# Optimization experiments

Hardware: AMD Instinct MI355X
Metric: run time of the kernel (lower is better)

Reference implementation:

```python
import jax, jax.numpy as jnp
import numpy as np

N = 50000       # nodes
E = 800000      # edges
D_IN, D_H, D_OUT = 64, 64, 32


def _glorot(key, fan_in, fan_out):
    lim = np.sqrt(6.0 / (fan_in + fan_out)).astype(np.float32)
    return jax.random.uniform(key, (fan_in, fan_out), jnp.float32, -lim, lim)


def setup_inputs() -> dict:
    key = jax.random.key(0)
    k = jax.random.split(key, 4)
    x = jax.random.normal(k[0], (N, D_IN), jnp.float32)
    edge_index = jax.random.randint(k[1], (2, E), 0, N, dtype=jnp.int64)
    W1 = _glorot(k[2], D_IN, D_H)
    b1 = jnp.zeros((D_H,), jnp.float32)
    W2 = _glorot(k[3], D_H, D_OUT)
    b2 = jnp.zeros((D_OUT,), jnp.float32)
    return {"x": x, "edge_index": edge_index, "W1": W1, "b1": b1, "W2": W2, "b2": b2}


def gcn_layer(x, W, b, src, dst, n):
    # PyG GCNConv: h = XW; add self-loops (weight 1); symmetric normalization
    # out[j] = sum_{i->j} h[i] / sqrt(deg(i) deg(j)) + h[j]/deg(j) + b
    h = x @ W                                           # [n, d_out]
    deg = jax.ops.segment_sum(jnp.ones((src.shape[0],), h.dtype), dst,
                              num_segments=n) + 1.0     # in-degree + self-loop
    dinv = jax.lax.rsqrt(deg)                           # deg >= 1
    norm = (dinv[src] * dinv[dst])[:, None]             # [E, 1]
    agg = jax.ops.segment_sum(h[src] * norm, dst, num_segments=n)
    # self-loop contribution: dinv[i]*dinv[i]*h[i]
    return agg + h * (dinv * dinv)[:, None] + b


def reference(x, edge_index, W1, b1, W2, b2):
    src, dst = edge_index[0], edge_index[1]
    h = gcn_layer(x, W1, b1, src, dst, N)
    h = jax.nn.relu(h)                                  # dropout is identity in eval mode
    return gcn_layer(h, W2, b2, src, dst, N)
```

## Files before the change

### kernel.cpp

```cpp
#include <hip/hip_runtime.h>
#include <hip/hip_fp16.h>
#include <cstddef>
#include <cstdint>

namespace {

constexpr int N  = 50000;
constexpr int E  = 800000;
constexpr int DH = 64;
constexpr int DO = 32;
constexpr int NB = (N + 255) / 256;
static_assert(N < 65536, "src packed as u16");
static_assert(NB <= 256, "phase-B single tile");

__device__ inline float bf2f(uint16_t u) {
    union { uint32_t u; float f; } c; c.u = (uint32_t)u << 16; return c.f;
}
__device__ inline uint16_t f2bf(float f) {
    union { float f; uint32_t u; } c; c.f = f;
    uint32_t r = c.u + 0x7FFFu + ((c.u >> 16) & 1u);
    return (uint16_t)(r >> 16);
}
__device__ inline void bf2x(uint32_t p, float& a, float& b) {
    union { uint32_t u; float f; } c0, c1;
    c0.u = p << 16; c1.u = p & 0xFFFF0000u;
    a = c0.f; b = c1.f;
}

__global__ void k_zero(int* __restrict__ cnt) {
    int i = blockIdx.x * blockDim.x + threadIdx.x;
    if (i < N) cnt[i] = 0;
}

__global__ void k_count(const int* __restrict__ dst, int* __restrict__ cnt,
                        int* __restrict__ rank) {
    int e = blockIdx.x * blockDim.x + threadIdx.x;
    if (e < E) rank[e] = atomicAdd(&cnt[dst[e]], 1);
}

__global__ void k_scanA(const int* __restrict__ cnt, int* __restrict__ incl,
                        int* __restrict__ bsum) {
    __shared__ int ts[256];
    const int t = threadIdx.x;
    const int i = blockIdx.x * 256 + t;
    const int v = (i < N) ? cnt[i] : 0;
    ts[t] = v;
    __syncthreads();
#pragma unroll
    for (int off = 1; off < 256; off <<= 1) {
        const int u = (t >= off) ? ts[t - off] : 0;
        __syncthreads();
        ts[t] += u;
        __syncthreads();
    }
    if (i < N) incl[i] = ts[t];
    if (t == 255) bsum[blockIdx.x] = ts[255];
}

__global__ void k_scanB(int* __restrict__ bsum) {
    __shared__ int ts[256];
    const int t = threadIdx.x;
    const int v = (t < NB) ? bsum[t] : 0;
    ts[t] = v;
    __syncthreads();
#pragma unroll
    for (int off = 1; off < 256; off <<= 1) {
        const int u = (t >= off) ? ts[t - off] : 0;
        __syncthreads();
        ts[t] += u;
        __syncthreads();
    }
    if (t < NB) bsum[t] = ts[t] - v;
}

__global__ void k_scanC(const int* __restrict__ cnt, const int* __restrict__ incl,
                        const int* __restrict__ bbase, int* __restrict__ rowptr,
                        float* __restrict__ dinv) {
    const int i = blockIdx.x * 256 + threadIdx.x;
    if (i >= N) return;
    const int c    = cnt[i];
    const int excl = bbase[blockIdx.x] + incl[i] - c;
    rowptr[i] = excl;
    dinv[i]   = rsqrtf((float)(c + 1));
    if (i == N - 1) rowptr[N] = excl + c;
}

__global__ void k_fill(const int* __restrict__ src, const int* __restrict__ dst,
                       const int* __restrict__ rank, const int* __restrict__ rowptr,
                       const float* __restrict__ dinv, uint32_t* __restrict__ epack) {
    int e = blockIdx.x * blockDim.x + threadIdx.x;
    if (e >= E) return;
    const int s = src[e], d = dst[e];
    const int pos = rowptr[d] + rank[e];
    const float wn = dinv[s] * dinv[d];
    const uint16_t hb = __half_as_ushort(__float2half(wn));
    epack[pos] = (uint32_t)s | ((uint32_t)hb << 16);
}

template <int DOUT, typename OutT>
__launch_bounds__(256)
__global__ void k_gemm(const float* __restrict__ X, const float* __restrict__ W,
                       OutT* __restrict__ H) {
    constexpr int CPT = DOUT / 16;
    static_assert(CPT == 4 || CPT == 2, "geometry");
    constexpr int XS = 68;
    __shared__ float Ws[64 * DOUT];
    __shared__ float Xs[64 * XS];

    const int tid = threadIdx.x;
    const int rowBase = blockIdx.x * 64;

    constexpr int WF4 = 64 * DOUT / 4;
#pragma unroll
    for (int i = 0; i < WF4 / 256; ++i) {
        const int q = tid + i * 256;
        reinterpret_cast<float4*>(Ws)[q] = reinterpret_cast<const float4*>(W)[q];
    }
#pragma unroll
    for (int i = 0; i < 4; ++i) {
        const int q   = tid + i * 256;
        const int row = q >> 4;
        const int kq  = q & 15;
        const int gr  = min(rowBase + row, N - 1);
        const float4 v = *reinterpret_cast<const float4*>(X + (size_t)gr * 64 + kq * 4);
        *reinterpret_cast<float4*>(&Xs[row * XS + kq * 4]) = v;
    }
    __syncthreads();

    const int rg = tid >> 4;
    const int cg = tid & 15;

    float acc[4][CPT];
#pragma unroll
    for (int r = 0; r < 4; ++r)
#pragma unroll
        for (int c = 0; c < CPT; ++c) acc[r][c] = 0.0f;

#pragma unroll
    for (int k4 = 0; k4 < 16; ++k4) {
        const int k = k4 * 4;
        float xr[4][4];
#pragma unroll
        for (int r = 0; r < 4; ++r) {
            const float4 v = *reinterpret_cast<const float4*>(&Xs[(rg * 4 + r) * XS + k]);
            xr[r][0] = v.x; xr[r][1] = v.y; xr[r][2] = v.z; xr[r][3] = v.w;
        }
#pragma unroll
        for (int i = 0; i < 4; ++i) {
            float wv[CPT];
            if constexpr (CPT == 4) {
                const float4 v = *reinterpret_cast<const float4*>(&Ws[(k + i) * DOUT + cg * 4]);
                wv[0] = v.x; wv[1] = v.y; wv[2] = v.z; wv[3] = v.w;
            } else {
                const float2 v = *reinterpret_cast<const float2*>(&Ws[(k + i) * DOUT + cg * 2]);
                wv[0] = v.x; wv[1] = v.y;
            }
#pragma unroll
            for (int r = 0; r < 4; ++r)
#pragma unroll
                for (int c = 0; c < CPT; ++c) acc[r][c] += xr[r][i] * wv[c];
        }
    }

#pragma unroll
    for (int r = 0; r < 4; ++r) {
        const int row = rowBase + rg * 4 + r;
        if (row < N) {
            if constexpr (sizeof(OutT) == 2) {
                uint2 o;
                o.x = (uint32_t)f2bf(acc[r][0]) | ((uint32_t)f2bf(acc[r][1]) << 16);
                o.y = (uint32_t)f2bf(acc[r][2]) | ((uint32_t)f2bf(acc[r][3]) << 16);
                *reinterpret_cast<uint2*>(&H[(size_t)row * DOUT + cg * 4]) = o;
            } else {
                float2 o; o.x = acc[r][0]; o.y = acc[r][1];
                *reinterpret_cast<float2*>(&H[(size_t)row * DOUT + cg * 2]) = o;
            }
        }
    }
}

__global__ void k_agg1(const int* __restrict__ rowptr, const uint32_t* __restrict__ epack,
                       const uint16_t* __restrict__ h1, const float* __restrict__ dinv,
                       const float* __restrict__ b1, float* __restrict__ y1) {
    const int gtid = blockIdx.x * blockDim.x + threadIdx.x;
    const int n    = gtid >> 6;
    const int lane = gtid & 63;
    if (n >= N) return;
    const int g  = lane >> 3;
    const int sl = lane & 7;
    const int beg = rowptr[n], end = rowptr[n + 1];

    float acc[8] = {0.f, 0.f, 0.f, 0.f, 0.f, 0.f, 0.f, 0.f};
    for (int j = beg; j < end; j += 8) {
        const int jj = j + g;
        int s = 0; float wn = 0.0f;
        if (jj < end) {
            const uint32_t w = epack[jj];
            s  = (int)(w & 0xFFFFu);
            wn = __half2float(__ushort_as_half((uint16_t)(w >> 16)));
        }
        const uint4 v = *reinterpret_cast<const uint4*>(h1 + (size_t)s * DH + sl * 8);
        float f0, f1;
        bf2x(v.x, f0, f1); acc[0] += wn * f0; acc[1] += wn * f1;
        bf2x(v.y, f0, f1); acc[2] += wn * f0; acc[3] += wn * f1;
        bf2x(v.z, f0, f1); acc[4] += wn * f0; acc[5] += wn * f1;
        bf2x(v.w, f0, f1); acc[6] += wn * f0; acc[7] += wn * f1;
    }
#pragma unroll
    for (int m = 8; m < 64; m <<= 1)
#pragma unroll
        for (int k = 0; k < 8; ++k) acc[k] += __shfl_xor(acc[k], m);

    if (g < 2) {
        const float di = dinv[n], d2 = di * di;
        const int fb = sl * 8 + g * 4;
        const uint2 sv = *reinterpret_cast<const uint2*>(h1 + (size_t)n * DH + fb);
        float s0, s1, s2, s3;
        bf2x(sv.x, s0, s1); bf2x(sv.y, s2, s3);
        const float4 bv = *reinterpret_cast<const float4*>(b1 + fb);
        float4 o;
        o.x = fmaxf(acc[g * 4 + 0] + s0 * d2 + bv.x, 0.f);
        o.y = fmaxf(acc[g * 4 + 1] + s1 * d2 + bv.y, 0.f);
        o.z = fmaxf(acc[g * 4 + 2] + s2 * d2 + bv.z, 0.f);
        o.w = fmaxf(acc[g * 4 + 3] + s3 * d2 + bv.w, 0.f);
        *reinterpret_cast<float4*>(y1 + (size_t)n * DH + fb) = o;
    }
}

__global__ void k_agg2(const int* __restrict__ rowptr, const uint32_t* __restrict__ epack,
                       const float* __restrict__ h2, const float* __restrict__ dinv,
                       const float* __restrict__ b2, float* __restrict__ out) {
    const int gtid = blockIdx.x * blockDim.x + threadIdx.x;
    const int n    = gtid >> 6;
    const int lane = gtid & 63;
    if (n >= N) return;
    const int g  = lane >> 3;
    const int sl = lane & 7;
    const int beg = rowptr[n], end = rowptr[n + 1];

    float acc[4] = {0.f, 0.f, 0.f, 0.f};
    for (int j = beg; j < end; j += 8) {
        const int jj = j + g;
        int s = 0; float wn = 0.0f;
        if (jj < end) {
            const uint32_t w = epack[jj];
            s  = (int)(w & 0xFFFFu);
            wn = __half2float(__ushort_as_half((uint16_t)(w >> 16)));
        }
        const float4 v = *reinterpret_cast<const float4*>(h2 + (size_t)s * DO + sl * 4);
        acc[0] += wn * v.x; acc[1] += wn * v.y;
        acc[2] += wn * v.z; acc[3] += wn * v.w;
    }
#pragma unroll
    for (int m = 8; m < 64; m <<= 1)
#pragma unroll
        for (int k = 0; k < 4; ++k) acc[k] += __shfl_xor(acc[k], m);

    if (g == 0) {
        const float di = dinv[n], d2 = di * di;
        const float4 sv = *reinterpret_cast<const float4*>(h2 + (size_t)n * DO + sl * 4);
        const float4 bv = *reinterpret_cast<const float4*>(b2 + sl * 4);
        float4 o;
        o.x = acc[0] + sv.x * d2 + bv.x;
        o.y = acc[1] + sv.y * d2 + bv.y;
        o.z = acc[2] + sv.z * d2 + bv.z;
        o.w = acc[3] + sv.w * d2 + bv.w;
        *reinterpret_cast<float4*>(out + (size_t)n * DO + sl * 4) = o;
    }
}

template <typename T>
T* alignp(char*& p, size_t count) {
    uintptr_t u = ((uintptr_t)p + 63) & ~(uintptr_t)63;
    p = (char*)(u + count * sizeof(T));
    return (T*)u;
}

}

extern "C" void kernel_launch(void* const* d_in, const int* in_sizes, int n_in,
                              void* d_out, int out_size, void* d_ws, size_t ws_size,
                              hipStream_t stream) {
    const float* x   = (const float*)d_in[0];
    const int*   ei  = (const int*)d_in[1];
    const float* W1  = (const float*)d_in[2];
    const float* b1  = (const float*)d_in[3];
    const float* W2  = (const float*)d_in[4];
    const float* b2  = (const float*)d_in[5];
    float* out = (float*)d_out;

    const int* src = ei;
    const int* dst = ei + E;

    char* p = (char*)d_ws;
    int*      cnt    = alignp<int>(p, N);
    int*      rowptr = alignp<int>(p, N + 1);
    int*      rank   = alignp<int>(p, E);
    float*    dinv   = alignp<float>(p, N);
    int*      incl   = alignp<int>(p, N);
    int*      bsum   = alignp<int>(p, NB);
    uint32_t* epack  = alignp<uint32_t>(p, E);
    uint16_t* h1     = alignp<uint16_t>(p, (size_t)N * DH);
    float*    y1     = alignp<float>(p, (size_t)N * DH);
    float*    h2     = (float*)h1;

    hipLaunchKernelGGL(k_zero, dim3((N + 255) / 256), dim3(256), 0, stream, cnt);
    hipLaunchKernelGGL(k_count, dim3((E + 255) / 256), dim3(256), 0, stream,
                       dst, cnt, rank);
    hipLaunchKernelGGL(k_scanA, dim3(NB), dim3(256), 0, stream, cnt, incl, bsum);
    hipLaunchKernelGGL(k_scanB, dim3(1), dim3(256), 0, stream, bsum);
    hipLaunchKernelGGL(k_scanC, dim3(NB), dim3(256), 0, stream, cnt, incl, bsum,
                       rowptr, dinv);
    hipLaunchKernelGGL(k_fill, dim3((E + 255) / 256), dim3(256), 0, stream,
                       src, dst, rank, rowptr, dinv, epack);
    hipLaunchKernelGGL((k_gemm<DH, uint16_t>), dim3((N + 63) / 64), dim3(256), 0, stream,
                       x, W1, h1);
    hipLaunchKernelGGL(k_agg1, dim3((N * 64 + 255) / 256), dim3(256), 0, stream,
                       rowptr, epack, h1, dinv, b1, y1);
    hipLaunchKernelGGL((k_gemm<DO, float>), dim3((N + 63) / 64), dim3(256), 0, stream,
                       y1, W2, h2);
    hipLaunchKernelGGL(k_agg2, dim3((N * 64 + 255) / 256), dim3(256), 0, stream,
                       rowptr, epack, h2, dinv, b2, out);
}
```

Measured before the change: 160.0 us.

## Fuse GEMM1 into count kernel, fuse layer-2 GEMM into agg1, bf16 h2

New measurement: 156.3 us. -2.3%, faster.

```diff
diff --git a/kernel.cpp b/kernel.cpp
--- a/kernel.cpp
+++ b/kernel.cpp
@@ -10,12 +10,14 @@
 constexpr int DH = 64;
 constexpr int DO = 32;
 constexpr int NB = (N + 255) / 256;
+constexpr int CB = (E + 255) / 256;
+constexpr int GB = (N + 63) / 64;
+constexpr int A1B = 3136;
+constexpr int NPW = 4;
 static_assert(N < 65536, "src packed as u16");
 static_assert(NB <= 256, "phase-B single tile");
-
-__device__ inline float bf2f(uint16_t u) {
-    union { uint32_t u; float f; } c; c.u = (uint32_t)u << 16; return c.f;
-}
+static_assert((size_t)A1B * 4 * NPW >= N, "agg1 coverage");
+
 __device__ inline uint16_t f2bf(float f) {
     union { float f; uint32_t u; } c; c.f = f;
     uint32_t r = c.u + 0x7FFFu + ((c.u >> 16) & 1u);
@@ -32,10 +34,76 @@
     if (i < N) cnt[i] = 0;
 }
 
-__global__ void k_count(const int* __restrict__ dst, int* __restrict__ cnt,
-                        int* __restrict__ rank) {
-    int e = blockIdx.x * blockDim.x + threadIdx.x;
-    if (e < E) rank[e] = atomicAdd(&cnt[dst[e]], 1);
+__launch_bounds__(256)
+__global__ void k_pre(const int* __restrict__ dst, int* __restrict__ cnt,
+                      int* __restrict__ rank, const float* __restrict__ X,
+                      const float* __restrict__ W1, uint16_t* __restrict__ h1) {
+    __shared__ float Ws[64 * DH];
+    __shared__ float Xs[64 * 68];
+
+    if (blockIdx.x < CB) {
+        const int e = blockIdx.x * 256 + threadIdx.x;
+        if (e < E) rank[e] = atomicAdd(&cnt[dst[e]], 1);
+        return;
+    }
+
+    const int tid = threadIdx.x;
+    const int rowBase = (blockIdx.x - CB) * 64;
+
+#pragma unroll
+    for (int i = 0; i < 4; ++i) {
+        const int q = tid + i * 256;
+        reinterpret_cast<float4*>(Ws)[q] = reinterpret_cast<const float4*>(W1)[q];
+    }
+#pragma unroll
+    for (int i = 0; i < 4; ++i) {
+        const int q   = tid + i * 256;
+        const int row = q >> 4;
+        const int kq  = q & 15;
+        const int gr  = min(rowBase + row, N - 1);
+        const float4 v = *reinterpret_cast<const float4*>(X + (size_t)gr * 64 + kq * 4);
+        *reinterpret_cast<float4*>(&Xs[row * 68 + kq * 4]) = v;
+    }
+    __syncthreads();
+
+    const int rg = tid >> 4;
+    const int cg = tid & 15;
+    float acc[4][4];
+#pragma unroll
+    for (int r = 0; r < 4; ++r)
+#pragma unroll
+        for (int c = 0; c < 4; ++c) acc[r][c] = 0.0f;
+
+#pragma unroll
+    for (int k4 = 0; k4 < 16; ++k4) {
+        const int k = k4 * 4;
+        float xr[4][4];
+#pragma unroll
+        for (int r = 0; r < 4; ++r) {
+            const float4 v = *reinterpret_cast<const float4*>(&Xs[(rg * 4 + r) * 68 + k]);
+            xr[r][0] = v.x; xr[r][1] = v.y; xr[r][2] = v.z; xr[r][3] = v.w;
+        }
+#pragma unroll
+        for (int i = 0; i < 4; ++i) {
+            const float4 v = *reinterpret_cast<const float4*>(&Ws[(k + i) * DH + cg * 4]);
+            const float wv[4] = {v.x, v.y, v.z, v.w};
+#pragma unroll
+            for (int r = 0; r < 4; ++r)
+#pragma unroll
+                for (int c = 0; c < 4; ++c) acc[r][c] += xr[r][i] * wv[c];
+        }
+    }
+
+#pragma unroll
+    for (int r = 0; r < 4; ++r) {
+        const int row = rowBase + rg * 4 + r;
+        if (row < N) {
+            uint2 o;
+            o.x = (uint32_t)f2bf(acc[r][0]) | ((uint32_t)f2bf(acc[r][1]) << 16);
+            o.y = (uint32_t)f2bf(acc[r][2]) | ((uint32_t)f2bf(acc[r][3]) << 16);
+            *reinterpret_cast<uint2*>(&h1[(size_t)row * DH + cg * 4]) = o;
+        }
+    }
 }
 
 __global__ void k_scanA(const int* __restrict__ cnt, int* __restrict__ incl,
@@ -97,101 +165,102 @@
     epack[pos] = (uint32_t)s | ((uint32_t)hb << 16);
 }
 
-template <int DOUT, typename OutT>
 __launch_bounds__(256)
-__global__ void k_gemm(const float* __restrict__ X, const float* __restrict__ W,
-                       OutT* __restrict__ H) {
-    constexpr int CPT = DOUT / 16;
-    static_assert(CPT == 4 || CPT == 2, "geometry");
-    constexpr int XS = 68;
-    __shared__ float Ws[64 * DOUT];
-    __shared__ float Xs[64 * XS];
-
-    const int tid = threadIdx.x;
-    const int rowBase = blockIdx.x * 64;
-
-    constexpr int WF4 = 64 * DOUT / 4;
-#pragma unroll
-    for (int i = 0; i < WF4 / 256; ++i) {
-        const int q = tid + i * 256;
-        reinterpret_cast<float4*>(Ws)[q] = reinterpret_cast<const float4*>(W)[q];
-    }
-#pragma unroll
-    for (int i = 0; i < 4; ++i) {
-        const int q   = tid + i * 256;
-        const int row = q >> 4;
-        const int kq  = q & 15;
-        const int gr  = min(rowBase + row, N - 1);
-        const float4 v = *reinterpret_cast<const float4*>(X + (size_t)gr * 64 + kq * 4);
-        *reinterpret_cast<float4*>(&Xs[row * XS + kq * 4]) = v;
-    }
-    __syncthreads();
-
-    const int rg = tid >> 4;
-    const int cg = tid & 15;
-
-    float acc[4][CPT];
-#pragma unroll
-    for (int r = 0; r < 4; ++r)
-#pragma unroll
-        for (int c = 0; c < CPT; ++c) acc[r][c] = 0.0f;
-
-#pragma unroll
-    for (int k4 = 0; k4 < 16; ++k4) {
-        const int k = k4 * 4;
-        float xr[4][4];
-#pragma unroll
-        for (int r = 0; r < 4; ++r) {
-            const float4 v = *reinterpret_cast<const float4*>(&Xs[(rg * 4 + r) * XS + k]);
-            xr[r][0] = v.x; xr[r][1] = v.y; xr[r][2] = v.z; xr[r][3] = v.w;
-        }
-#pragma unroll
-        for (int i = 0; i < 4; ++i) {
-            float wv[CPT];
-            if constexpr (CPT == 4) {
-                const float4 v = *reinterpret_cast<const float4*>(&Ws[(k + i) * DOUT + cg * 4]);
-                wv[0] = v.x; wv[1] = v.y; wv[2] = v.z; wv[3] = v.w;
-            } else {
-                const float2 v = *reinterpret_cast<const float2*>(&Ws[(k + i) * DOUT + cg * 2]);
-                wv[0] = v.x; wv[1] = v.y;
-            }
-#pragma unroll
-            for (int r = 0; r < 4; ++r)
-#pragma unroll
-                for (int c = 0; c < CPT; ++c) acc[r][c] += xr[r][i] * wv[c];
-        }
-    }
-
-#pragma unroll
-    for (int r = 0; r < 4; ++r) {
-        const int row = rowBase + rg * 4 + r;
-        if (row < N) {
-            if constexpr (sizeof(OutT) == 2) {
-                uint2 o;
-                o.x = (uint32_t)f2bf(acc[r][0]) | ((uint32_t)f2bf(acc[r][1]) << 16);
-                o.y = (uint32_t)f2bf(acc[r][2]) | ((uint32_t)f2bf(acc[r][3]) << 16);
-                *reinterpret_cast<uint2*>(&H[(size_t)row * DOUT + cg * 4]) = o;
-            } else {
-                float2 o; o.x = acc[r][0]; o.y = acc[r][1];
-                *reinterpret_cast<float2*>(&H[(size_t)row * DOUT + cg * 2]) = o;
-            }
-        }
-    }
-}
-
 __global__ void k_agg1(const int* __restrict__ rowptr, const uint32_t* __restrict__ epack,
                        const uint16_t* __restrict__ h1, const float* __restrict__ dinv,
-                       const float* __restrict__ b1, float* __restrict__ y1) {
+                       const float* __restrict__ W2, const float* __restrict__ b1,
+                       uint16_t* __restrict__ h2) {
+    const int wid  = (blockIdx.x * 256 + threadIdx.x) >> 6;
+    const int lane = threadIdx.x & 63;
+    const int g  = lane >> 3;
+    const int sl = lane & 7;
+
+    float w2r[8][4];
+#pragma unroll
+    for (int k = 0; k < 8; ++k) {
+        const float4 v = *reinterpret_cast<const float4*>(W2 + (size_t)(sl * 8 + k) * DO + g * 4);
+        w2r[k][0] = v.x; w2r[k][1] = v.y; w2r[k][2] = v.z; w2r[k][3] = v.w;
+    }
+    float b1r[8];
+    {
+        const float4 a = *reinterpret_cast<const float4*>(b1 + sl * 8);
+        const float4 b = *reinterpret_cast<const float4*>(b1 + sl * 8 + 4);
+        b1r[0] = a.x; b1r[1] = a.y; b1r[2] = a.z; b1r[3] = a.w;
+        b1r[4] = b.x; b1r[5] = b.y; b1r[6] = b.z; b1r[7] = b.w;
+    }
+
+    const int nBeg = wid * NPW;
+    for (int ni = 0; ni < NPW; ++ni) {
+        const int n = nBeg + ni;
+        if (n >= N) return;
+        const int beg = rowptr[n], end = rowptr[n + 1];
+
+        float acc[8] = {0.f, 0.f, 0.f, 0.f, 0.f, 0.f, 0.f, 0.f};
+        for (int j = beg; j < end; j += 8) {
+            const int jj = j + g;
+            int s = 0; float wn = 0.0f;
+            if (jj < end) {
+                const uint32_t w = epack[jj];
+                s  = (int)(w & 0xFFFFu);
+                wn = __half2float(__ushort_as_half((uint16_t)(w >> 16)));
+            }
+            const uint4 v = *reinterpret_cast<const uint4*>(h1 + (size_t)s * DH + sl * 8);
+            float f0, f1;
+            bf2x(v.x, f0, f1); acc[0] += wn * f0; acc[1] += wn * f1;
+            bf2x(v.y, f0, f1); acc[2] += wn * f0; acc[3] += wn * f1;
+            bf2x(v.z, f0, f1); acc[4] += wn * f0; acc[5] += wn * f1;
+            bf2x(v.w, f0, f1); acc[6] += wn * f0; acc[7] += wn * f1;
+        }
+#pragma unroll
+        for (int m = 8; m < 64; m <<= 1)
+#pragma unroll
+            for (int k = 0; k < 8; ++k) acc[k] += __shfl_xor(acc[k], m);
+
+        const float di = dinv[n], d2 = di * di;
+        const uint4 sv = *reinterpret_cast<const uint4*>(h1 + (size_t)n * DH + sl * 8);
+        float y[8];
+        {
+            float f0, f1;
+            bf2x(sv.x, f0, f1); y[0] = acc[0] + f0 * d2; y[1] = acc[1] + f1 * d2;
+            bf2x(sv.y, f0, f1); y[2] = acc[2] + f0 * d2; y[3] = acc[3] + f1 * d2;
+            bf2x(sv.z, f0, f1); y[4] = acc[4] + f0 * d2; y[5] = acc[5] + f1 * d2;
+            bf2x(sv.w, f0, f1); y[6] = acc[6] + f0 * d2; y[7] = acc[7] + f1 * d2;
+        }
+#pragma unroll
+        for (int k = 0; k < 8; ++k) y[k] = fmaxf(y[k] + b1r[k], 0.0f);
+
+        float o[4] = {0.f, 0.f, 0.f, 0.f};
+#pragma unroll
+        for (int k = 0; k < 8; ++k)
+#pragma unroll
+            for (int c = 0; c < 4; ++c) o[c] += y[k] * w2r[k][c];
+#pragma unroll
+        for (int m = 1; m < 8; m <<= 1)
+#pragma unroll
+            for (int c = 0; c < 4; ++c) o[c] += __shfl_xor(o[c], m);
+
+        if (sl == 0) {
+            uint2 pk;
+            pk.x = (uint32_t)f2bf(o[0]) | ((uint32_t)f2bf(o[1]) << 16);
+            pk.y = (uint32_t)f2bf(o[2]) | ((uint32_t)f2bf(o[3]) << 16);
+            *reinterpret_cast<uint2*>(h2 + (size_t)n * DO + g * 4) = pk;
+        }
+    }
+}
+
+__global__ void k_agg2(const int* __restrict__ rowptr, const uint32_t* __restrict__ epack,
+                       const uint16_t* __restrict__ h2, const float* __restrict__ dinv,
+                       const float* __restrict__ b2, float* __restrict__ out) {
     const int gtid = blockIdx.x * blockDim.x + threadIdx.x;
     const int n    = gtid >> 6;
     const int lane = gtid & 63;
     if (n >= N) return;
-    const int g  = lane >> 3;
-    const int sl = lane & 7;
+    const int g  = lane >> 2;
+    const int sl = lane & 3;
     const int beg = rowptr[n], end = rowptr[n + 1];
 
     float acc[8] = {0.f, 0.f, 0.f, 0.f, 0.f, 0.f, 0.f, 0.f};
-    for (int j = beg; j < end; j += 8) {
+    for (int j = beg; j < end; j += 16) {
         const int jj = j + g;
         int s = 0; float wn = 0.0f;
         if (jj < end) {
@@ -199,7 +268,7 @@
             s  = (int)(w & 0xFFFFu);
             wn = __half2float(__ushort_as_half((uint16_t)(w >> 16)));
         }
-        const uint4 v = *reinterpret_cast<const uint4*>(h1 + (size_t)s * DH + sl * 8);
+        const uint4 v = *reinterpret_cast<const uint4*>(h2 + (size_t)s * DO + sl * 8);
         float f0, f1;
         bf2x(v.x, f0, f1); acc[0] += wn * f0; acc[1] += wn * f1;
         bf2x(v.y, f0, f1); acc[2] += wn * f0; acc[3] += wn * f1;
@@ -207,65 +276,23 @@
         bf2x(v.w, f0, f1); acc[6] += wn * f0; acc[7] += wn * f1;
     }
 #pragma unroll
-    for (int m = 8; m < 64; m <<= 1)
+    for (int m = 4; m < 64; m <<= 1)
 #pragma unroll
         for (int k = 0; k < 8; ++k) acc[k] += __shfl_xor(acc[k], m);
 
     if (g < 2) {
         const float di = dinv[n], d2 = di * di;
         const int fb = sl * 8 + g * 4;
-        const uint2 sv = *reinterpret_cast<const uint2*>(h1 + (size_t)n * DH + fb);
+        const uint2 sv = *reinterpret_cast<const uint2*>(h2 + (size_t)n * DO + fb);
         float s0, s1, s2, s3;
         bf2x(sv.x, s0, s1); bf2x(sv.y, s2, s3);
-        const float4 bv = *reinterpret_cast<const float4*>(b1 + fb);
+        const float4 bv = *reinterpret_cast<const float4*>(b2 + fb);
         float4 o;
-        o.x = fmaxf(acc[g * 4 + 0] + s0 * d2 + bv.x, 0.f);
-        o.y = fmaxf(acc[g * 4 + 1] + s1 * d2 + bv.y, 0.f);
-        o.z = fmaxf(acc[g * 4 + 2] + s2 * d2 + bv.z, 0.f);
-        o.w = fmaxf(acc[g * 4 + 3] + s3 * d2 + bv.w, 0.f);
-        *reinterpret_cast<float4*>(y1 + (size_t)n * DH + fb) = o;
-    }
-}
-
-__global__ void k_agg2(const int* __restrict__ rowptr, const uint32_t* __restrict__ epack,
-                       const float* __restrict__ h2, const float* __restrict__ dinv,
-                       const float* __restrict__ b2, float* __restrict__ out) {
-    const int gtid = blockIdx.x * blockDim.x + threadIdx.x;
-    const int n    = gtid >> 6;
-    const int lane = gtid & 63;
-    if (n >= N) return;
-    const int g  = lane >> 3;
-    const int sl = lane & 7;
-    const int beg = rowptr[n], end = rowptr[n + 1];
-
-    float acc[4] = {0.f, 0.f, 0.f, 0.f};
-    for (int j = beg; j < end; j += 8) {
-        const int jj = j + g;
-        int s = 0; float wn = 0.0f;
-        if (jj < end) {
-            const uint32_t w = epack[jj];
-            s  = (int)(w & 0xFFFFu);
-            wn = __half2float(__ushort_as_half((uint16_t)(w >> 16)));
-        }
-        const float4 v = *reinterpret_cast<const float4*>(h2 + (size_t)s * DO + sl * 4);
-        acc[0] += wn * v.x; acc[1] += wn * v.y;
-        acc[2] += wn * v.z; acc[3] += wn * v.w;
-    }
-#pragma unroll
-    for (int m = 8; m < 64; m <<= 1)
-#pragma unroll
-        for (int k = 0; k < 4; ++k) acc[k] += __shfl_xor(acc[k], m);
-
-    if (g == 0) {
-        const float di = dinv[n], d2 = di * di;
-        const float4 sv = *reinterpret_cast<const float4*>(h2 + (size_t)n * DO + sl * 4);
-        const float4 bv = *reinterpret_cast<const float4*>(b2 + sl * 4);
-        float4 o;
-        o.x = acc[0] + sv.x * d2 + bv.x;
-        o.y = acc[1] + sv.y * d2 + bv.y;
-        o.z = acc[2] + sv.z * d2 + bv.z;
-        o.w = acc[3] + sv.w * d2 + bv.w;
-        *reinterpret_cast<float4*>(out + (size_t)n * DO + sl * 4) = o;
+        o.x = acc[g * 4 + 0] + s0 * d2 + bv.x;
+        o.y = acc[g * 4 + 1] + s1 * d2 + bv.y;
+        o.z = acc[g * 4 + 2] + s2 * d2 + bv.z;
+        o.w = acc[g * 4 + 3] + s3 * d2 + bv.w;
+        *reinterpret_cast<float4*>(out + (size_t)n * DO + fb) = o;
     }
 }
 
@@ -301,24 +328,19 @@
     int*      bsum   = alignp<int>(p, NB);
     uint32_t* epack  = alignp<uint32_t>(p, E);
     uint16_t* h1     = alignp<uint16_t>(p, (size_t)N * DH);
-    float*    y1     = alignp<float>(p, (size_t)N * DH);
-    float*    h2     = (float*)h1;
+    uint16_t* h2     = alignp<uint16_t>(p, (size_t)N * DO);
 
     hipLaunchKernelGGL(k_zero, dim3((N + 255) / 256), dim3(256), 0, stream, cnt);
-    hipLaunchKernelGGL(k_count, dim3((E + 255) / 256), dim3(256), 0, stream,
-                       dst, cnt, rank);
+    hipLaunchKernelGGL(k_pre, dim3(CB + GB), dim3(256), 0, stream,
+                       dst, cnt, rank, x, W1, h1);
     hipLaunchKernelGGL(k_scanA, dim3(NB), dim3(256), 0, stream, cnt, incl, bsum);
     hipLaunchKernelGGL(k_scanB, dim3(1), dim3(256), 0, stream, bsum);
     hipLaunchKernelGGL(k_scanC, dim3(NB), dim3(256), 0, stream, cnt, incl, bsum,
                        rowptr, dinv);
     hipLaunchKernelGGL(k_fill, dim3((E + 255) / 256), dim3(256), 0, stream,
                        src, dst, rank, rowptr, dinv, epack);
-    hipLaunchKernelGGL((k_gemm<DH, uint16_t>), dim3((N + 63) / 64), dim3(256), 0, stream,
-                       x, W1, h1);
-    hipLaunchKernelGGL(k_agg1, dim3((N * 64 + 255) / 256), dim3(256), 0, stream,
-                       rowptr, epack, h1, dinv, b1, y1);
-    hipLaunchKernelGGL((k_gemm<DO, float>), dim3((N + 63) / 64), dim3(256), 0, stream,
-                       y1, W2, h2);
+    hipLaunchKernelGGL(k_agg1, dim3(A1B), dim3(256), 0, stream,
+                       rowptr, epack, h1, dinv, W2, b1, h2);
     hipLaunchKernelGGL(k_agg2, dim3((N * 64 + 255) / 256), dim3(256), 0, stream,
                        rowptr, epack, h2, dinv, b2, out);
 }
```
